# Performance work log

Hardware: AMD Instinct MI355X
Metric: run time of the kernel (lower is better)

Reference implementation:

```python
import jax, jax.numpy as jnp
import numpy as np

HEADS = 16  # init_kwargs['heads']


def setup_inputs() -> dict:
    key = jax.random.key(0)
    k1, k2, k3, k4, k5, k6 = jax.random.split(key, 6)
    N, L, E = 2, 2048, 1024
    return {
        "values": jax.random.normal(k1, (N, L, E), dtype=jnp.float32),
        "key": jax.random.normal(k2, (N, L, E), dtype=jnp.float32),
        "query": jax.random.normal(k3, (N, L, E), dtype=jnp.float32),
        "mask": jax.random.randint(k4, (N, 1, L, L), 0, 2, dtype=jnp.int32),
        # fc_out: Linear(heads*head_dim=E, E) with bias
        "W_out": jax.random.normal(k5, (E, E), dtype=jnp.float32) / np.sqrt(E),
        "b_out": jax.random.normal(k6, (E,), dtype=jnp.float32) * 0.01,
    }


def reference(values, key, query, mask, W_out, b_out):
    N, Lq, E = query.shape
    Lk = key.shape[1]
    H = HEADS
    D = E // H  # head_dim = 64
    q = query.reshape(N, Lq, H, D)
    k = key.reshape(N, Lk, H, D)
    v = values.reshape(N, Lk, H, D)
    # energy: (N, H, Q, K)
    energy = jnp.einsum("nqhd,nkhd->nhqk", q, k)
    # masked_fill BEFORE scaling, as in the original
    energy = jnp.where(mask == 0, jnp.float32(-1e20), energy)
    attn = jax.nn.softmax(energy / np.float32(np.sqrt(D)), axis=3)
    out = jnp.einsum("nhqk,nkhd->nqhd", attn, v).reshape(N, Lq, H * D)
    return out @ W_out.T + b_out
```

## Files before the change

### kernel.cpp

```cpp
#include <hip/hip_runtime.h>

#define L_SEQ  2048
#define EMB    1024
#define NHEAD  16
#define HDIM   64
#define NBATCH 2
#define NT     (L_SEQ / 64)

typedef unsigned short u16;
typedef unsigned int   u32;
typedef unsigned long long u64;
typedef short bf16x8 __attribute__((ext_vector_type(8)));
typedef float f32x4  __attribute__((ext_vector_type(4)));
typedef int   i32x4  __attribute__((ext_vector_type(4)));

static __device__ __forceinline__ u16 f2bf(float x) {
    union { float f; unsigned u; } a; a.f = x;
    unsigned r = a.u + 0x7FFFu + ((a.u >> 16) & 1u);
    return (u16)(r >> 16);
}
static __device__ __forceinline__ void cvt8(const float4& a, const float4& b, u16* o, float s) {
    o[0]=f2bf(a.x*s); o[1]=f2bf(a.y*s); o[2]=f2bf(a.z*s); o[3]=f2bf(a.w*s);
    o[4]=f2bf(b.x*s); o[5]=f2bf(b.y*s); o[6]=f2bf(b.z*s); o[7]=f2bf(b.w*s);
}

static __device__ __forceinline__ u32 cvt_pk_bf16(float lo, float hi) {
    u32 r;
    asm("v_cvt_pk_bf16_f32 %0, %1, %2" : "=v"(r) : "v"(lo), "v"(hi));
    return r;
}
static __device__ __forceinline__ void permswap32(u32 &x, u32 &y) {
    asm("v_permlane32_swap_b32 %0, %1" : "+v"(x), "+v"(y));
}
static __device__ __forceinline__ void permswap16(u32 &x, u32 &y) {
    asm("v_permlane16_swap_b32 %0, %1" : "+v"(x), "+v"(y));
}

static __device__ __forceinline__ void lds_barrier() {
    asm volatile("s_waitcnt lgkmcnt(0)" ::: "memory");
    __builtin_amdgcn_s_barrier();
    __builtin_amdgcn_sched_barrier(0);
}

__global__ __launch_bounds__(256)
void prep_fused(const float* __restrict__ Qg, const float* __restrict__ Kg,
                const float* __restrict__ Vg, const int* __restrict__ Mg,
                const float* __restrict__ Wg,
                u16* __restrict__ Qb, u16* __restrict__ Kb, u16* __restrict__ Vt,
                u64* __restrict__ maskp, u16* __restrict__ Wb)
{
    const int bid = blockIdx.x;
    const int tid = threadIdx.x;
    __shared__ u16 Vl2[64][72];

    if (bid < 1024) {
        const int wave = tid >> 6;
        const int lane = tid & 63;
        const int row  = bid * 4 + wave;
        const int* mp = Mg + (size_t)row * L_SEQ + lane;
        u64* op = maskp + (size_t)row * NT;
        for (int tt = 0; tt < NT; ++tt) {
            u64 b = __ballot(mp[tt * 64] != 0);
            if (lane == 0) op[tt] = b;
        }
    } else if (bid < 2048) {
        const int b  = bid - 1024;
        const int tt = b & 31, hh = (b >> 5) & 15, nn = b >> 9;
        const int row = tid >> 2;
        const int dc  = (tid & 3) * 16;

        const size_t gin = ((size_t)(nn * L_SEQ) + tt * 64 + row) * EMB + hh * HDIM + dc;

        {
            const float qs = 0.125f * 1.44269504f;
            u16 o[16];
            cvt8(*(const float4*)(Qg + gin),     *(const float4*)(Qg + gin + 4),  o,     qs);
            cvt8(*(const float4*)(Qg + gin + 8), *(const float4*)(Qg + gin + 12), o + 8, qs);
            *(uint4*)(Qb + gin)     = *(const uint4*)o;
            *(uint4*)(Qb + gin + 8) = *(const uint4*)&o[8];
        }
        {
            u16 o[16];
            cvt8(*(const float4*)(Kg + gin),     *(const float4*)(Kg + gin + 4),  o,     1.f);
            cvt8(*(const float4*)(Kg + gin + 8), *(const float4*)(Kg + gin + 12), o + 8, 1.f);
            size_t ko = ((size_t)(nn * NHEAD + hh) * L_SEQ + tt * 64 + row) * HDIM + dc;
            *(uint4*)(Kb + ko)     = *(const uint4*)o;
            *(uint4*)(Kb + ko + 8) = *(const uint4*)&o[8];
        }
        {
            u16 o[16];
            cvt8(*(const float4*)(Vg + gin),     *(const float4*)(Vg + gin + 4),  o,     1.f);
            cvt8(*(const float4*)(Vg + gin + 8), *(const float4*)(Vg + gin + 12), o + 8, 1.f);
            #pragma unroll
            for (int j = 0; j < 16; ++j) Vl2[dc + j][row] = o[j];
        }
        __syncthreads();
        {
            const int d  = tid >> 2;
            const int kc = (tid & 3) * 16;
            size_t vo = ((size_t)(nn * NHEAD + hh) * HDIM + d) * L_SEQ + tt * 64 + kc;
            *(uint4*)(Vt + vo)     = *(const uint4*)&Vl2[d][kc];
            *(uint4*)(Vt + vo + 8) = *(const uint4*)&Vl2[d][kc + 8];
        }
    } else {
        int i = ((bid - 2048) * 256 + tid) * 8;
        float4 a = *(const float4*)(Wg + i);
        float4 b4 = *(const float4*)(Wg + i + 4);
        u16 o[8];
        cvt8(a, b4, o, 1.f);
        *(uint4*)(Wb + i) = *(const uint4*)o;
    }
}

static __device__ __forceinline__ void pv_step(
    const u32 (&Dwp)[2][8], const u16 (&Vb)[64][72],
    f32x4 (&acc)[2][4], int l16, int quad)
{
    #pragma unroll
    for (int kc = 0; kc < 2; ++kc) {
        bf16x8 pf[2];
        #pragma unroll
        for (int qs = 0; qs < 2; ++qs) {
            u32 b0 = Dwp[qs][4 * kc + 0], b2 = Dwp[qs][4 * kc + 2];
            permswap32(b0, b2); permswap16(b0, b2);
            u32 b1 = Dwp[qs][4 * kc + 1], b3 = Dwp[qs][4 * kc + 3];
            permswap32(b1, b3); permswap16(b1, b3);
            union { i32x4 i; bf16x8 v; } pu;
            pu.i[0] = (int)b0; pu.i[1] = (int)b1; pu.i[2] = (int)b2; pu.i[3] = (int)b3;
            pf[qs] = pu.v;
        }
        #pragma unroll
        for (int dc = 0; dc < 4; ++dc) {
            bf16x8 vf = *(const bf16x8*)&Vb[dc * 16 + l16][kc * 32 + quad * 8];
            acc[0][dc] = __builtin_amdgcn_mfma_f32_16x16x32_bf16(vf, pf[0], acc[0][dc], 0, 0, 0);
            acc[1][dc] = __builtin_amdgcn_mfma_f32_16x16x32_bf16(vf, pf[1], acc[1][dc], 0, 0, 0);
        }
    }
}

static __device__ __forceinline__ void attn_tile(
    int t, int kbuf, int vprev, int kw, int vw,
    u32 (&Dwc)[2][8], u32 (&Dwp)[2][8],
    u16 (&Kl)[2][64][72], u16 (&Vl)[4][64][72],
    const bf16x8 (&qf)[2][2], f32x4 (&acc)[2][4], float (&ls)[2][4],
    uint4& kr0, uint4& kr1, uint4& vr0, uint4& vr1,
    u64& mr0, u64& mr1,
    const u16* kbase, const u16* vbase, const u64* mbase, int mqs,
    int srow, int scol, int l16, int quad)
{
    if (t < NT - 1) {
        *(uint4*)&Kl[kw][srow][scol]     = kr0;
        *(uint4*)&Kl[kw][srow][scol + 8] = kr1;
        *(uint4*)&Vl[vw][srow][scol]     = vr0;
        *(uint4*)&Vl[vw][srow][scol + 8] = vr1;
    }
    u64 mcur0 = mr0, mcur1 = mr1;
    if (t < NT - 1) { mr0 = mbase[t + 1]; mr1 = mbase[mqs + t + 1]; }
    if (t < NT - 2) {
        const u16* kp = kbase + (size_t)((t + 2) * 64 + srow) * HDIM + scol;
        const u16* vp = vbase + (size_t)srow * L_SEQ + (t + 2) * 64 + scol;
        kr0 = *(const uint4*)kp;  kr1 = *(const uint4*)(kp + 8);
        vr0 = *(const uint4*)vp;  vr1 = *(const uint4*)(vp + 8);
    }

    const int sh = quad * 4;
    u32 mlo0 = (u32)mcur0 >> sh, mhi0 = (u32)(mcur0 >> 32) >> sh;
    u32 mlo1 = (u32)mcur1 >> sh, mhi1 = (u32)(mcur1 >> 32) >> sh;
    #pragma unroll
    for (int cc = 0; cc < 4; ++cc) {
        bf16x8 k0 = *(const bf16x8*)&Kl[kbuf][cc * 16 + l16][quad * 8];
        bf16x8 k1 = *(const bf16x8*)&Kl[kbuf][cc * 16 + l16][32 + quad * 8];
        f32x4 z0; z0[0]=0.f; z0[1]=0.f; z0[2]=0.f; z0[3]=0.f;
        f32x4 z1 = z0;
        z0 = __builtin_amdgcn_mfma_f32_16x16x32_bf16(k0, qf[0][0], z0, 0, 0, 0);
        z0 = __builtin_amdgcn_mfma_f32_16x16x32_bf16(k1, qf[0][1], z0, 0, 0, 0);
        z1 = __builtin_amdgcn_mfma_f32_16x16x32_bf16(k0, qf[1][0], z1, 0, 0, 0);
        z1 = __builtin_amdgcn_mfma_f32_16x16x32_bf16(k1, qf[1][1], z1, 0, 0, 0);

        #pragma unroll
        for (int qs = 0; qs < 2; ++qs) {
            const f32x4& z = (qs == 0) ? z0 : z1;
            u32 w = (cc < 2) ? ((qs == 0) ? mlo0 : mlo1)
                             : ((qs == 0) ? mhi0 : mhi1);
            float pv[4];
            #pragma unroll
            for (int r = 0; r < 4; ++r) {
                const int pos = (cc & 1) * 16 + r;
                int sm = (int)(w << (31 - pos)) >> 31;
                float p = __builtin_amdgcn_exp2f(z[r]);
                p = __int_as_float(__float_as_int(p) & sm);
                ls[qs][r] += p;
                pv[r] = p;
            }
            Dwc[qs][2 * cc]     = cvt_pk_bf16(pv[0], pv[1]);
            Dwc[qs][2 * cc + 1] = cvt_pk_bf16(pv[2], pv[3]);
        }
    }

    pv_step(Dwp, Vl[vprev], acc, l16, quad);

    lds_barrier();
}

__global__ __launch_bounds__(256, 2)
void attn_kernel(const u16* __restrict__ Qb, const u16* __restrict__ Kb,
                 const u16* __restrict__ Vt, const u64* __restrict__ maskp,
                 u16* __restrict__ Og)
{
    const int i    = blockIdx.x;
    const int x    = i & 7;
    const int s    = i >> 3;
    const int g    = ((s >> 4) << 3) + x;
    const int qblk = s & 15;
    const int h    = g & 15;
    const int n    = g >> 4;

    const int tid  = threadIdx.x;
    const int wave = tid >> 6;
    const int lane = tid & 63;
    const int l16  = lane & 15;
    const int quad = lane >> 4;

    __shared__ u16 Kl[2][64][72];
    __shared__ u16 Vl[4][64][72];

    const int q0 = qblk * 128 + wave * 32;

    bf16x8 qf[2][2];
    #pragma unroll
    for (int qs = 0; qs < 2; ++qs) {
        const u16* qp = Qb + ((size_t)(n * L_SEQ) + q0 + qs * 16 + l16) * EMB + h * HDIM;
        qf[qs][0] = *(const bf16x8*)(qp + quad * 8);
        qf[qs][1] = *(const bf16x8*)(qp + 32 + quad * 8);
    }

    f32x4 acc[2][4];
    #pragma unroll
    for (int qs = 0; qs < 2; ++qs)
        #pragma unroll
        for (int c = 0; c < 4; ++c)
            #pragma unroll
            for (int r = 0; r < 4; ++r) acc[qs][c][r] = 0.f;
    float ls[2][4];
    #pragma unroll
    for (int qs = 0; qs < 2; ++qs)
        #pragma unroll
        for (int r = 0; r < 4; ++r) ls[qs][r] = 0.f;

    u32 DwA[2][8], DwB[2][8];
    #pragma unroll
    for (int qs = 0; qs < 2; ++qs)
        #pragma unroll
        for (int ii = 0; ii < 8; ++ii) { DwA[qs][ii] = 0u; DwB[qs][ii] = 0u; }

    const u16* kbase = Kb + (size_t)(n * NHEAD + h) * L_SEQ * HDIM;
    const u16* vbase = Vt + (size_t)(n * NHEAD + h) * HDIM * L_SEQ;
    const u64* mbase = maskp + ((size_t)(n * L_SEQ) + q0 + l16) * NT;
    const int  mqs   = 16 * NT;

    const int srow = tid >> 2;
    const int scol = (tid & 3) * 16;

    uint4 kr0, kr1, vr0, vr1;
    u64 mr0, mr1;

    {
        const u16* kp = kbase + (size_t)srow * HDIM + scol;
        const u16* vp = vbase + (size_t)srow * L_SEQ + scol;
        kr0 = *(const uint4*)kp;  kr1 = *(const uint4*)(kp + 8);
        vr0 = *(const uint4*)vp;  vr1 = *(const uint4*)(vp + 8);
    }
    *(uint4*)&Kl[0][srow][scol]     = kr0;
    *(uint4*)&Kl[0][srow][scol + 8] = kr1;
    *(uint4*)&Vl[0][srow][scol]     = vr0;
    *(uint4*)&Vl[0][srow][scol + 8] = vr1;
    {
        u32* vz = (u32*)&Vl[3][0][0];
        #pragma unroll
        for (int ii = 0; ii < 9; ++ii) vz[tid + ii * 256] = 0u;
    }
    {
        const u16* kp = kbase + (size_t)(64 + srow) * HDIM + scol;
        const u16* vp = vbase + (size_t)srow * L_SEQ + 64 + scol;
        kr0 = *(const uint4*)kp;  kr1 = *(const uint4*)(kp + 8);
        vr0 = *(const uint4*)vp;  vr1 = *(const uint4*)(vp + 8);
    }
    mr0 = mbase[0];
    mr1 = mbase[mqs];
    __syncthreads();

    for (int j = 0; j < 8; ++j) {
        const int t = j * 4;
        attn_tile(t + 0, 0, 3, 1, 1, DwA, DwB, Kl, Vl, qf, acc, ls,
                  kr0, kr1, vr0, vr1, mr0, mr1, kbase, vbase, mbase, mqs,
                  srow, scol, l16, quad);
        attn_tile(t + 1, 1, 0, 0, 2, DwB, DwA, Kl, Vl, qf, acc, ls,
                  kr0, kr1, vr0, vr1, mr0, mr1, kbase, vbase, mbase, mqs,
                  srow, scol, l16, quad);
        attn_tile(t + 2, 0, 1, 1, 3, DwA, DwB, Kl, Vl, qf, acc, ls,
                  kr0, kr1, vr0, vr1, mr0, mr1, kbase, vbase, mbase, mqs,
                  srow, scol, l16, quad);
        attn_tile(t + 3, 1, 2, 0, 0, DwB, DwA, Kl, Vl, qf, acc, ls,
                  kr0, kr1, vr0, vr1, mr0, mr1, kbase, vbase, mbase, mqs,
                  srow, scol, l16, quad);
    }

    pv_step(DwB, Vl[3], acc, l16, quad);

    #pragma unroll
    for (int qs = 0; qs < 2; ++qs) {
        float sm = (ls[qs][0] + ls[qs][1]) + (ls[qs][2] + ls[qs][3]);
        sm += __shfl_xor(sm, 16);
        sm += __shfl_xor(sm, 32);
        float inv = 1.f / sm;

        u16* op = Og + ((size_t)(n * L_SEQ) + q0 + qs * 16 + l16) * EMB + h * HDIM + quad * 4;
        #pragma unroll
        for (int dc = 0; dc < 4; ++dc) {
            u32 u0 = cvt_pk_bf16(acc[qs][dc][0] * inv, acc[qs][dc][1] * inv);
            u32 u1 = cvt_pk_bf16(acc[qs][dc][2] * inv, acc[qs][dc][3] * inv);
            uint2 st; st.x = u0; st.y = u1;
            *(uint2*)(op + dc * 16) = st;
        }
    }
}

__global__ __launch_bounds__(512)
void out_gemm(const u16* __restrict__ A, const u16* __restrict__ B,
              const float* __restrict__ bias, float* __restrict__ out)
{
    const int i  = blockIdx.x;
    const int bn = i & 7;
    const int bm = i >> 3;

    const int tid = threadIdx.x;
    const int wave = tid >> 6;
    const int lane = tid & 63;
    const int l16  = lane & 15;
    const int quad = lane >> 4;
    const int wr = wave >> 2;
    const int wc = wave & 3;

    __shared__ u16 Al[2][128][72];
    __shared__ u16 Bl[2][128][72];

    f32x4 acc[4][2];
    #pragma unroll
    for (int ii = 0; ii < 4; ++ii)
        #pragma unroll
        for (int j = 0; j < 2; ++j)
            #pragma unroll
            for (int r = 0; r < 4; ++r) acc[ii][j][r] = 0.f;

    const int srow = tid >> 2;
    const int kc   = (tid & 3) * 16;

    const u16* ap = A + (size_t)(bm * 128 + srow) * EMB + kc;
    const u16* bp = B + (size_t)(bn * 128 + srow) * EMB + kc;

    uint4 ar0 = *(const uint4*)ap,        ar1 = *(const uint4*)(ap + 8);
    uint4 br0 = *(const uint4*)bp,        br1 = *(const uint4*)(bp + 8);

    #pragma unroll 4
    for (int s = 0; s < 16; ++s) {
        const int b = s & 1;
        *(uint4*)&Al[b][srow][kc]     = ar0;
        *(uint4*)&Al[b][srow][kc + 8] = ar1;
        *(uint4*)&Bl[b][srow][kc]     = br0;
        *(uint4*)&Bl[b][srow][kc + 8] = br1;
        if (s < 15) {
            const int k0 = (s + 1) * 64;
            ar0 = *(const uint4*)(ap + k0);      ar1 = *(const uint4*)(ap + k0 + 8);
            br0 = *(const uint4*)(bp + k0);      br1 = *(const uint4*)(bp + k0 + 8);
        }
        lds_barrier();

        #pragma unroll
        for (int kk = 0; kk < 2; ++kk) {
            bf16x8 af[4], bfr[2];
            #pragma unroll
            for (int ii = 0; ii < 4; ++ii)
                af[ii] = *(const bf16x8*)&Al[b][wr * 64 + ii * 16 + l16][kk * 32 + quad * 8];
            #pragma unroll
            for (int j = 0; j < 2; ++j)
                bfr[j] = *(const bf16x8*)&Bl[b][wc * 32 + j * 16 + l16][kk * 32 + quad * 8];
            #pragma unroll
            for (int ii = 0; ii < 4; ++ii)
                #pragma unroll
                for (int j = 0; j < 2; ++j)
                    acc[ii][j] = __builtin_amdgcn_mfma_f32_16x16x32_bf16(af[ii], bfr[j], acc[ii][j], 0, 0, 0);
        }
    }

    #pragma unroll
    for (int j = 0; j < 2; ++j) {
        int col = bn * 128 + wc * 32 + j * 16 + l16;
        float bv = bias[col];
        #pragma unroll
        for (int ii = 0; ii < 4; ++ii) {
            int row0 = bm * 128 + wr * 64 + ii * 16 + quad * 4;
            #pragma unroll
            for (int r = 0; r < 4; ++r)
                out[(size_t)(row0 + r) * EMB + col] = acc[ii][j][r] + bv;
        }
    }
}

extern "C" void kernel_launch(void* const* d_in, const int* in_sizes, int n_in,
                              void* d_out, int out_size, void* d_ws, size_t ws_size,
                              hipStream_t stream)
{
    const float* Vg = (const float*)d_in[0];
    const float* Kg = (const float*)d_in[1];
    const float* Qg = (const float*)d_in[2];
    const int*   Mg = (const int*)d_in[3];
    const float* Wg = (const float*)d_in[4];
    const float* Bg = (const float*)d_in[5];
    float* Og = (float*)d_out;

    const size_t QKV = (size_t)NBATCH * L_SEQ * EMB;
    char* ws = (char*)d_ws;
    u16* attn_ws = (u16*)ws;
    u16* Wb      = (u16*)(ws + QKV * 2);
    u16* Qb      = (u16*)(ws + QKV * 2 + 2 * 1024 * 1024);
    u16* Kb      = Qb + QKV;
    u16* Vt      = Kb + QKV;
    u64* maskp   = (u64*)(Vt + QKV);

    prep_fused<<<dim3(2560), 256, 0, stream>>>(Qg, Kg, Vg, Mg, Wg,
                                               Qb, Kb, Vt, maskp, Wb);

    attn_kernel<<<dim3(512), 256, 0, stream>>>(Qb, Kb, Vt, maskp, attn_ws);

    out_gemm<<<dim3(256), 512, 0, stream>>>(attn_ws, Wb, Bg, Og);
}
```

Measured before the change: 207.8 us.

## Split key range across two wave groups in attention kernel with LDS reduction

The attention kernel now runs 512 threads per block. Two groups of four waves each process alternating 64-key tiles for the same 128 queries, then combine their partial accumulators and row sums through LDS before normalising. The old software-pipelined tile helper, which overlapped the P·V step with the next tile's QK^T, is replaced by a simpler loop that loads two tiles per iteration into a four-slot K/V ring. The P·V MFMA section is wrapped in s_setprio. This is meant to raise wave-level parallelism and latency hiding, at the cost of losing the explicit intra-wave overlap and adding a final cross-group reduction.

```diff
diff --git a/kernel.cpp b/kernel.cpp
--- a/kernel.cpp
+++ b/kernel.cpp
@@ -116,6 +116,7 @@
     const u32 (&Dwp)[2][8], const u16 (&Vb)[64][72],
     f32x4 (&acc)[2][4], int l16, int quad)
 {
+    __builtin_amdgcn_s_setprio(1);
     #pragma unroll
     for (int kc = 0; kc < 2; ++kc) {
         bf16x8 pf[2];
@@ -136,73 +137,10 @@
             acc[1][dc] = __builtin_amdgcn_mfma_f32_16x16x32_bf16(vf, pf[1], acc[1][dc], 0, 0, 0);
         }
     }
-}
-
-static __device__ __forceinline__ void attn_tile(
-    int t, int kbuf, int vprev, int kw, int vw,
-    u32 (&Dwc)[2][8], u32 (&Dwp)[2][8],
-    u16 (&Kl)[2][64][72], u16 (&Vl)[4][64][72],
-    const bf16x8 (&qf)[2][2], f32x4 (&acc)[2][4], float (&ls)[2][4],
-    uint4& kr0, uint4& kr1, uint4& vr0, uint4& vr1,
-    u64& mr0, u64& mr1,
-    const u16* kbase, const u16* vbase, const u64* mbase, int mqs,
-    int srow, int scol, int l16, int quad)
-{
-    if (t < NT - 1) {
-        *(uint4*)&Kl[kw][srow][scol]     = kr0;
-        *(uint4*)&Kl[kw][srow][scol + 8] = kr1;
-        *(uint4*)&Vl[vw][srow][scol]     = vr0;
-        *(uint4*)&Vl[vw][srow][scol + 8] = vr1;
-    }
-    u64 mcur0 = mr0, mcur1 = mr1;
-    if (t < NT - 1) { mr0 = mbase[t + 1]; mr1 = mbase[mqs + t + 1]; }
-    if (t < NT - 2) {
-        const u16* kp = kbase + (size_t)((t + 2) * 64 + srow) * HDIM + scol;
-        const u16* vp = vbase + (size_t)srow * L_SEQ + (t + 2) * 64 + scol;
-        kr0 = *(const uint4*)kp;  kr1 = *(const uint4*)(kp + 8);
-        vr0 = *(const uint4*)vp;  vr1 = *(const uint4*)(vp + 8);
-    }
-
-    const int sh = quad * 4;
-    u32 mlo0 = (u32)mcur0 >> sh, mhi0 = (u32)(mcur0 >> 32) >> sh;
-    u32 mlo1 = (u32)mcur1 >> sh, mhi1 = (u32)(mcur1 >> 32) >> sh;
-    #pragma unroll
-    for (int cc = 0; cc < 4; ++cc) {
-        bf16x8 k0 = *(const bf16x8*)&Kl[kbuf][cc * 16 + l16][quad * 8];
-        bf16x8 k1 = *(const bf16x8*)&Kl[kbuf][cc * 16 + l16][32 + quad * 8];
-        f32x4 z0; z0[0]=0.f; z0[1]=0.f; z0[2]=0.f; z0[3]=0.f;
-        f32x4 z1 = z0;
-        z0 = __builtin_amdgcn_mfma_f32_16x16x32_bf16(k0, qf[0][0], z0, 0, 0, 0);
-        z0 = __builtin_amdgcn_mfma_f32_16x16x32_bf16(k1, qf[0][1], z0, 0, 0, 0);
-        z1 = __builtin_amdgcn_mfma_f32_16x16x32_bf16(k0, qf[1][0], z1, 0, 0, 0);
-        z1 = __builtin_amdgcn_mfma_f32_16x16x32_bf16(k1, qf[1][1], z1, 0, 0, 0);
-
-        #pragma unroll
-        for (int qs = 0; qs < 2; ++qs) {
-            const f32x4& z = (qs == 0) ? z0 : z1;
-            u32 w = (cc < 2) ? ((qs == 0) ? mlo0 : mlo1)
-                             : ((qs == 0) ? mhi0 : mhi1);
-            float pv[4];
-            #pragma unroll
-            for (int r = 0; r < 4; ++r) {
-                const int pos = (cc & 1) * 16 + r;
-                int sm = (int)(w << (31 - pos)) >> 31;
-                float p = __builtin_amdgcn_exp2f(z[r]);
-                p = __int_as_float(__float_as_int(p) & sm);
-                ls[qs][r] += p;
-                pv[r] = p;
-            }
-            Dwc[qs][2 * cc]     = cvt_pk_bf16(pv[0], pv[1]);
-            Dwc[qs][2 * cc + 1] = cvt_pk_bf16(pv[2], pv[3]);
-        }
-    }
-
-    pv_step(Dwp, Vl[vprev], acc, l16, quad);
-
-    lds_barrier();
-}
-
-__global__ __launch_bounds__(256, 2)
+    __builtin_amdgcn_s_setprio(0);
+}
+
+__global__ __launch_bounds__(512, 4)
 void attn_kernel(const u16* __restrict__ Qb, const u16* __restrict__ Kb,
                  const u16* __restrict__ Vt, const u64* __restrict__ maskp,
                  u16* __restrict__ Og)
@@ -217,14 +155,16 @@
 
     const int tid  = threadIdx.x;
     const int wave = tid >> 6;
+    const int qg   = wave & 3;
+    const int kh   = wave >> 2;
     const int lane = tid & 63;
     const int l16  = lane & 15;
     const int quad = lane >> 4;
 
-    __shared__ u16 Kl[2][64][72];
+    __shared__ u16 Kl[4][64][72];
     __shared__ u16 Vl[4][64][72];
 
-    const int q0 = qblk * 128 + wave * 32;
+    const int q0 = qblk * 128 + qg * 32;
 
     bf16x8 qf[2][2];
     #pragma unroll
@@ -247,80 +187,133 @@
         #pragma unroll
         for (int r = 0; r < 4; ++r) ls[qs][r] = 0.f;
 
-    u32 DwA[2][8], DwB[2][8];
-    #pragma unroll
-    for (int qs = 0; qs < 2; ++qs)
-        #pragma unroll
-        for (int ii = 0; ii < 8; ++ii) { DwA[qs][ii] = 0u; DwB[qs][ii] = 0u; }
-
     const u16* kbase = Kb + (size_t)(n * NHEAD + h) * L_SEQ * HDIM;
     const u16* vbase = Vt + (size_t)(n * NHEAD + h) * HDIM * L_SEQ;
     const u64* mbase = maskp + ((size_t)(n * L_SEQ) + q0 + l16) * NT;
     const int  mqs   = 16 * NT;
 
-    const int srow = tid >> 2;
-    const int scol = (tid & 3) * 16;
-
-    uint4 kr0, kr1, vr0, vr1;
-    u64 mr0, mr1;
-
-    {
-        const u16* kp = kbase + (size_t)srow * HDIM + scol;
-        const u16* vp = vbase + (size_t)srow * L_SEQ + scol;
-        kr0 = *(const uint4*)kp;  kr1 = *(const uint4*)(kp + 8);
-        vr0 = *(const uint4*)vp;  vr1 = *(const uint4*)(vp + 8);
-    }
-    *(uint4*)&Kl[0][srow][scol]     = kr0;
-    *(uint4*)&Kl[0][srow][scol + 8] = kr1;
-    *(uint4*)&Vl[0][srow][scol]     = vr0;
-    *(uint4*)&Vl[0][srow][scol + 8] = vr1;
-    {
-        u32* vz = (u32*)&Vl[3][0][0];
-        #pragma unroll
-        for (int ii = 0; ii < 9; ++ii) vz[tid + ii * 256] = 0u;
-    }
-    {
-        const u16* kp = kbase + (size_t)(64 + srow) * HDIM + scol;
-        const u16* vp = vbase + (size_t)srow * L_SEQ + 64 + scol;
-        kr0 = *(const uint4*)kp;  kr1 = *(const uint4*)(kp + 8);
-        vr0 = *(const uint4*)vp;  vr1 = *(const uint4*)(vp + 8);
-    }
-    mr0 = mbase[0];
-    mr1 = mbase[mqs];
+    const int sr = tid >> 3;
+    const int sc = (tid & 7) * 8;
+
+    *(uint4*)&Kl[0][sr][sc] = *(const uint4*)(kbase + (size_t)sr * HDIM + sc);
+    *(uint4*)&Vl[0][sr][sc] = *(const uint4*)(vbase + (size_t)sr * L_SEQ + sc);
+    *(uint4*)&Kl[1][sr][sc] = *(const uint4*)(kbase + (size_t)(64 + sr) * HDIM + sc);
+    *(uint4*)&Vl[1][sr][sc] = *(const uint4*)(vbase + (size_t)sr * L_SEQ + 64 + sc);
+    u64 mr0 = mbase[kh];
+    u64 mr1 = mbase[mqs + kh];
     __syncthreads();
 
-    for (int j = 0; j < 8; ++j) {
-        const int t = j * 4;
-        attn_tile(t + 0, 0, 3, 1, 1, DwA, DwB, Kl, Vl, qf, acc, ls,
-                  kr0, kr1, vr0, vr1, mr0, mr1, kbase, vbase, mbase, mqs,
-                  srow, scol, l16, quad);
-        attn_tile(t + 1, 1, 0, 0, 2, DwB, DwA, Kl, Vl, qf, acc, ls,
-                  kr0, kr1, vr0, vr1, mr0, mr1, kbase, vbase, mbase, mqs,
-                  srow, scol, l16, quad);
-        attn_tile(t + 2, 0, 1, 1, 3, DwA, DwB, Kl, Vl, qf, acc, ls,
-                  kr0, kr1, vr0, vr1, mr0, mr1, kbase, vbase, mbase, mqs,
-                  srow, scol, l16, quad);
-        attn_tile(t + 3, 1, 2, 0, 0, DwB, DwA, Kl, Vl, qf, acc, ls,
-                  kr0, kr1, vr0, vr1, mr0, mr1, kbase, vbase, mbase, mqs,
-                  srow, scol, l16, quad);
-    }
-
-    pv_step(DwB, Vl[3], acc, l16, quad);
-
-    #pragma unroll
-    for (int qs = 0; qs < 2; ++qs) {
-        float sm = (ls[qs][0] + ls[qs][1]) + (ls[qs][2] + ls[qs][3]);
-        sm += __shfl_xor(sm, 16);
-        sm += __shfl_xor(sm, 32);
-        float inv = 1.f / sm;
-
-        u16* op = Og + ((size_t)(n * L_SEQ) + q0 + qs * 16 + l16) * EMB + h * HDIM + quad * 4;
-        #pragma unroll
-        for (int dc = 0; dc < 4; ++dc) {
-            u32 u0 = cvt_pk_bf16(acc[qs][dc][0] * inv, acc[qs][dc][1] * inv);
-            u32 u1 = cvt_pk_bf16(acc[qs][dc][2] * inv, acc[qs][dc][3] * inv);
-            uint2 st; st.x = u0; st.y = u1;
-            *(uint2*)(op + dc * 16) = st;
+    #pragma unroll 2
+    for (int u = 0; u < 16; ++u) {
+        uint4 ka, va, kb2, vb2;
+        if (u < 15) {
+            const int t2 = 2 * u + 2, t3 = 2 * u + 3;
+            ka  = *(const uint4*)(kbase + (size_t)(t2 * 64 + sr) * HDIM + sc);
+            va  = *(const uint4*)(vbase + (size_t)sr * L_SEQ + t2 * 64 + sc);
+            kb2 = *(const uint4*)(kbase + (size_t)(t3 * 64 + sr) * HDIM + sc);
+            vb2 = *(const uint4*)(vbase + (size_t)sr * L_SEQ + t3 * 64 + sc);
+        }
+        const u64 mcur0 = mr0, mcur1 = mr1;
+        if (u < 15) {
+            mr0 = mbase[2 * u + 2 + kh];
+            mr1 = mbase[mqs + 2 * u + 2 + kh];
+        }
+
+        const int t  = 2 * u + kh;
+        const int rs = t & 3;
+
+        const int sh = quad * 4;
+        u32 mlo0 = (u32)mcur0 >> sh, mhi0 = (u32)(mcur0 >> 32) >> sh;
+        u32 mlo1 = (u32)mcur1 >> sh, mhi1 = (u32)(mcur1 >> 32) >> sh;
+
+        u32 Dw[2][8];
+        #pragma unroll
+        for (int cc = 0; cc < 4; ++cc) {
+            bf16x8 k0 = *(const bf16x8*)&Kl[rs][cc * 16 + l16][quad * 8];
+            bf16x8 k1 = *(const bf16x8*)&Kl[rs][cc * 16 + l16][32 + quad * 8];
+            f32x4 z0; z0[0]=0.f; z0[1]=0.f; z0[2]=0.f; z0[3]=0.f;
+            f32x4 z1 = z0;
+            z0 = __builtin_amdgcn_mfma_f32_16x16x32_bf16(k0, qf[0][0], z0, 0, 0, 0);
+            z0 = __builtin_amdgcn_mfma_f32_16x16x32_bf16(k1, qf[0][1], z0, 0, 0, 0);
+            z1 = __builtin_amdgcn_mfma_f32_16x16x32_bf16(k0, qf[1][0], z1, 0, 0, 0);
+            z1 = __builtin_amdgcn_mfma_f32_16x16x32_bf16(k1, qf[1][1], z1, 0, 0, 0);
+
+            #pragma unroll
+            for (int qs = 0; qs < 2; ++qs) {
+                const f32x4& z = (qs == 0) ? z0 : z1;
+                u32 w = (cc < 2) ? ((qs == 0) ? mlo0 : mlo1)
+                                 : ((qs == 0) ? mhi0 : mhi1);
+                float pv[4];
+                #pragma unroll
+                for (int r = 0; r < 4; ++r) {
+                    const int pos = (cc & 1) * 16 + r;
+                    int sm = (int)(w << (31 - pos)) >> 31;
+                    float p = __builtin_amdgcn_exp2f(z[r]);
+                    p = __int_as_float(__float_as_int(p) & sm);
+                    ls[qs][r] += p;
+                    pv[r] = p;
+                }
+                Dw[qs][2 * cc]     = cvt_pk_bf16(pv[0], pv[1]);
+                Dw[qs][2 * cc + 1] = cvt_pk_bf16(pv[2], pv[3]);
+            }
+        }
+
+        pv_step(Dw, Vl[rs], acc, l16, quad);
+
+        if (u < 15) {
+            const int s2 = (2 * u + 2) & 3, s3 = (2 * u + 3) & 3;
+            *(uint4*)&Kl[s2][sr][sc] = ka;
+            *(uint4*)&Vl[s2][sr][sc] = va;
+            *(uint4*)&Kl[s3][sr][sc] = kb2;
+            *(uint4*)&Vl[s3][sr][sc] = vb2;
+        }
+        lds_barrier();
+    }
+
+    float lsA[2];
+    lsA[0] = (ls[0][0] + ls[0][1]) + (ls[0][2] + ls[0][3]);
+    lsA[1] = (ls[1][0] + ls[1][1]) + (ls[1][2] + ls[1][3]);
+
+    float* cb = (float*)&Kl[0][0][0];
+    const int cbase = (qg * 64 + lane) * 34;
+    if (kh == 1) {
+        #pragma unroll
+        for (int qs = 0; qs < 2; ++qs)
+            #pragma unroll
+            for (int dc = 0; dc < 4; ++dc)
+                #pragma unroll
+                for (int r = 0; r < 4; ++r)
+                    cb[cbase + qs * 16 + dc * 4 + r] = acc[qs][dc][r];
+        cb[cbase + 32] = lsA[0];
+        cb[cbase + 33] = lsA[1];
+    }
+    __syncthreads();
+    if (kh == 0) {
+        #pragma unroll
+        for (int qs = 0; qs < 2; ++qs)
+            #pragma unroll
+            for (int dc = 0; dc < 4; ++dc)
+                #pragma unroll
+                for (int r = 0; r < 4; ++r)
+                    acc[qs][dc][r] += cb[cbase + qs * 16 + dc * 4 + r];
+        lsA[0] += cb[cbase + 32];
+        lsA[1] += cb[cbase + 33];
+
+        #pragma unroll
+        for (int qs = 0; qs < 2; ++qs) {
+            float sm = lsA[qs];
+            sm += __shfl_xor(sm, 16);
+            sm += __shfl_xor(sm, 32);
+            float inv = 1.f / sm;
+
+            u16* op = Og + ((size_t)(n * L_SEQ) + q0 + qs * 16 + l16) * EMB + h * HDIM + quad * 4;
+            #pragma unroll
+            for (int dc = 0; dc < 4; ++dc) {
+                u32 u0 = cvt_pk_bf16(acc[qs][dc][0] * inv, acc[qs][dc][1] * inv);
+                u32 u1 = cvt_pk_bf16(acc[qs][dc][2] * inv, acc[qs][dc][3] * inv);
+                uint2 st; st.x = u0; st.y = u1;
+                *(uint2*)(op + dc * 16) = st;
+            }
         }
     }
 }
@@ -430,7 +423,7 @@
     prep_fused<<<dim3(2560), 256, 0, stream>>>(Qg, Kg, Vg, Mg, Wg,
                                                Qb, Kb, Vt, maskp, Wb);
 
-    attn_kernel<<<dim3(512), 256, 0, stream>>>(Qb, Kb, Vt, maskp, attn_ws);
+    attn_kernel<<<dim3(512), 512, 0, stream>>>(Qb, Kb, Vt, maskp, attn_ws);
 
     out_gemm<<<dim3(256), 512, 0, stream>>>(attn_ws, Wb, Bg, Og);
 }
```

Measured after the change: 399.4 us. +92.2%, slower.

## Fuse Q and W bf16 conversion into consumers and raise MFMA priority

Applied to the files above, without the earlier changes.

The separate prep-stage conversions of Q (with softmax scale) and W_out to bf16 are removed. Q is now loaded as fp32 and converted inside attn_kernel, and W is converted while being staged into LDS in out_gemm. This saves a bf16 write and read round trip and shrinks the prep grid. In exchange, out_gemm reads twice the bytes for B and converts W repeatedly across the M tiles. s_setprio is also raised around the PV MFMA block.

```diff
diff --git a/kernel.cpp b/kernel.cpp
--- a/kernel.cpp
+++ b/kernel.cpp
@@ -43,11 +43,10 @@
 }
 
 __global__ __launch_bounds__(256)
-void prep_fused(const float* __restrict__ Qg, const float* __restrict__ Kg,
-                const float* __restrict__ Vg, const int* __restrict__ Mg,
-                const float* __restrict__ Wg,
-                u16* __restrict__ Qb, u16* __restrict__ Kb, u16* __restrict__ Vt,
-                u64* __restrict__ maskp, u16* __restrict__ Wb)
+void prep_fused(const float* __restrict__ Kg, const float* __restrict__ Vg,
+                const int* __restrict__ Mg,
+                u16* __restrict__ Kb, u16* __restrict__ Vt,
+                u64* __restrict__ maskp)
 {
     const int bid = blockIdx.x;
     const int tid = threadIdx.x;
@@ -63,7 +62,7 @@
             u64 b = __ballot(mp[tt * 64] != 0);
             if (lane == 0) op[tt] = b;
         }
-    } else if (bid < 2048) {
+    } else {
         const int b  = bid - 1024;
         const int tt = b & 31, hh = (b >> 5) & 15, nn = b >> 9;
         const int row = tid >> 2;
@@ -71,14 +70,6 @@
 
         const size_t gin = ((size_t)(nn * L_SEQ) + tt * 64 + row) * EMB + hh * HDIM + dc;
 
-        {
-            const float qs = 0.125f * 1.44269504f;
-            u16 o[16];
-            cvt8(*(const float4*)(Qg + gin),     *(const float4*)(Qg + gin + 4),  o,     qs);
-            cvt8(*(const float4*)(Qg + gin + 8), *(const float4*)(Qg + gin + 12), o + 8, qs);
-            *(uint4*)(Qb + gin)     = *(const uint4*)o;
-            *(uint4*)(Qb + gin + 8) = *(const uint4*)&o[8];
-        }
         {
             u16 o[16];
             cvt8(*(const float4*)(Kg + gin),     *(const float4*)(Kg + gin + 4),  o,     1.f);
@@ -102,13 +93,6 @@
             *(uint4*)(Vt + vo)     = *(const uint4*)&Vl2[d][kc];
             *(uint4*)(Vt + vo + 8) = *(const uint4*)&Vl2[d][kc + 8];
         }
-    } else {
-        int i = ((bid - 2048) * 256 + tid) * 8;
-        float4 a = *(const float4*)(Wg + i);
-        float4 b4 = *(const float4*)(Wg + i + 4);
-        u16 o[8];
-        cvt8(a, b4, o, 1.f);
-        *(uint4*)(Wb + i) = *(const uint4*)o;
     }
 }
 
@@ -116,6 +100,7 @@
     const u32 (&Dwp)[2][8], const u16 (&Vb)[64][72],
     f32x4 (&acc)[2][4], int l16, int quad)
 {
+    __builtin_amdgcn_s_setprio(1);
     #pragma unroll
     for (int kc = 0; kc < 2; ++kc) {
         bf16x8 pf[2];
@@ -136,6 +121,7 @@
             acc[1][dc] = __builtin_amdgcn_mfma_f32_16x16x32_bf16(vf, pf[1], acc[1][dc], 0, 0, 0);
         }
     }
+    __builtin_amdgcn_s_setprio(0);
 }
 
 static __device__ __forceinline__ void attn_tile(
@@ -203,7 +189,7 @@
 }
 
 __global__ __launch_bounds__(256, 2)
-void attn_kernel(const u16* __restrict__ Qb, const u16* __restrict__ Kb,
+void attn_kernel(const float* __restrict__ Qg, const u16* __restrict__ Kb,
                  const u16* __restrict__ Vt, const u64* __restrict__ maskp,
                  u16* __restrict__ Og)
 {
@@ -227,11 +213,20 @@
     const int q0 = qblk * 128 + wave * 32;
 
     bf16x8 qf[2][2];
-    #pragma unroll
-    for (int qs = 0; qs < 2; ++qs) {
-        const u16* qp = Qb + ((size_t)(n * L_SEQ) + q0 + qs * 16 + l16) * EMB + h * HDIM;
-        qf[qs][0] = *(const bf16x8*)(qp + quad * 8);
-        qf[qs][1] = *(const bf16x8*)(qp + 32 + quad * 8);
+    {
+        const float qscale = 0.125f * 1.44269504f;
+        #pragma unroll
+        for (int qs = 0; qs < 2; ++qs) {
+            const float* qp = Qg + ((size_t)(n * L_SEQ) + q0 + qs * 16 + l16) * EMB + h * HDIM;
+            #pragma unroll
+            for (int half = 0; half < 2; ++half) {
+                float4 a = *(const float4*)(qp + half * 32 + quad * 8);
+                float4 b = *(const float4*)(qp + half * 32 + quad * 8 + 4);
+                u16 o[8];
+                cvt8(a, b, o, qscale);
+                qf[qs][half] = *(const bf16x8*)o;
+            }
+        }
     }
 
     f32x4 acc[2][4];
@@ -326,7 +321,7 @@
 }
 
 __global__ __launch_bounds__(512)
-void out_gemm(const u16* __restrict__ A, const u16* __restrict__ B,
+void out_gemm(const u16* __restrict__ A, const float* __restrict__ W,
               const float* __restrict__ bias, float* __restrict__ out)
 {
     const int i  = blockIdx.x;
@@ -355,23 +350,30 @@
     const int srow = tid >> 2;
     const int kc   = (tid & 3) * 16;
 
-    const u16* ap = A + (size_t)(bm * 128 + srow) * EMB + kc;
-    const u16* bp = B + (size_t)(bn * 128 + srow) * EMB + kc;
-
-    uint4 ar0 = *(const uint4*)ap,        ar1 = *(const uint4*)(ap + 8);
-    uint4 br0 = *(const uint4*)bp,        br1 = *(const uint4*)(bp + 8);
+    const u16*  ap = A + (size_t)(bm * 128 + srow) * EMB + kc;
+    const float* bp = W + (size_t)(bn * 128 + srow) * EMB + kc;
+
+    uint4  ar0 = *(const uint4*)ap,      ar1 = *(const uint4*)(ap + 8);
+    float4 br0 = *(const float4*)bp,     br1 = *(const float4*)(bp + 4);
+    float4 br2 = *(const float4*)(bp + 8), br3 = *(const float4*)(bp + 12);
 
     #pragma unroll 4
     for (int s = 0; s < 16; ++s) {
         const int b = s & 1;
         *(uint4*)&Al[b][srow][kc]     = ar0;
         *(uint4*)&Al[b][srow][kc + 8] = ar1;
-        *(uint4*)&Bl[b][srow][kc]     = br0;
-        *(uint4*)&Bl[b][srow][kc + 8] = br1;
+        {
+            u16 ob[16];
+            cvt8(br0, br1, ob,     1.f);
+            cvt8(br2, br3, ob + 8, 1.f);
+            *(uint4*)&Bl[b][srow][kc]     = *(const uint4*)ob;
+            *(uint4*)&Bl[b][srow][kc + 8] = *(const uint4*)&ob[8];
+        }
         if (s < 15) {
             const int k0 = (s + 1) * 64;
-            ar0 = *(const uint4*)(ap + k0);      ar1 = *(const uint4*)(ap + k0 + 8);
-            br0 = *(const uint4*)(bp + k0);      br1 = *(const uint4*)(bp + k0 + 8);
+            ar0 = *(const uint4*)(ap + k0);       ar1 = *(const uint4*)(ap + k0 + 8);
+            br0 = *(const float4*)(bp + k0);      br1 = *(const float4*)(bp + k0 + 4);
+            br2 = *(const float4*)(bp + k0 + 8);  br3 = *(const float4*)(bp + k0 + 12);
         }
         lds_barrier();
 
@@ -421,16 +423,13 @@
     const size_t QKV = (size_t)NBATCH * L_SEQ * EMB;
     char* ws = (char*)d_ws;
     u16* attn_ws = (u16*)ws;
-    u16* Wb      = (u16*)(ws + QKV * 2);
-    u16* Qb      = (u16*)(ws + QKV * 2 + 2 * 1024 * 1024);
-    u16* Kb      = Qb + QKV;
+    u16* Kb      = (u16*)(ws + QKV * 2);
     u16* Vt      = Kb + QKV;
     u64* maskp   = (u64*)(Vt + QKV);
 
-    prep_fused<<<dim3(2560), 256, 0, stream>>>(Qg, Kg, Vg, Mg, Wg,
-                                               Qb, Kb, Vt, maskp, Wb);
-
-    attn_kernel<<<dim3(512), 256, 0, stream>>>(Qb, Kb, Vt, maskp, attn_ws);
-
-    out_gemm<<<dim3(256), 512, 0, stream>>>(attn_ws, Wb, Bg, Og);
-}
+    prep_fused<<<dim3(2048), 256, 0, stream>>>(Kg, Vg, Mg, Kb, Vt, maskp);
+
+    attn_kernel<<<dim3(512), 256, 0, stream>>>(Qg, Kb, Vt, maskp, attn_ws);
+
+    out_gemm<<<dim3(256), 512, 0, stream>>>(attn_ws, Wg, Bg, Og);
+}
```

Result: no change. 207.8 us (+0.0%).
